# Kernel tuning notes

Hardware: AMD Instinct MI355X
Metric: run time of the kernel (lower is better)

The kernel has to match this reference:

```python
import jax, jax.numpy as jnp
import numpy as np

EMBED = 384; HEADS = 12; POINTS = 9; LAYERS = 2
KFG = 20; KBG = 50; NITER = 10
B = 4; H = 64; W = 64


def _layer_norm(x, g, b, eps=1e-5):
    m = x.mean(-1, keepdims=True)
    v = ((x - m) ** 2).mean(-1, keepdims=True)
    return (x - m) * jax.lax.rsqrt(v + eps) * g + b


def _sine_pos(pad, C):
    # pad [B,H,W], 1.0 = padded. SinePositionalEncoding(num_feats=C//2, normalize=True)
    nf = C // 2
    not_m = 1.0 - pad
    y = jnp.cumsum(not_m, axis=1)
    x = jnp.cumsum(not_m, axis=2)
    eps = 1e-6; sc = 2.0 * np.pi
    y = y / (y[:, -1:, :] + eps) * sc
    x = x / (x[:, :, -1:] + eps) * sc
    t = jnp.arange(nf, dtype=jnp.float32)
    dim_t = 10000.0 ** (2.0 * jnp.floor(t / 2.0) / nf)
    px = x[..., None] / dim_t
    py = y[..., None] / dim_t
    def inter(p):
        b_, h_, w_, _ = p.shape
        return jnp.stack((jnp.sin(p[..., 0::2]), jnp.cos(p[..., 1::2])), -1).reshape(b_, h_, w_, nf)
    pos = jnp.concatenate([inter(py), inter(px)], -1)  # [B,H,W,C]
    return pos.reshape(pad.shape[0], -1, C)


def _kmeans(x, w, K, n_iter):
    # masked Lloyd k-means. x [B,N,C], w [B,N] in {0,1} (1 = member of the group)
    Bq, N, C = x.shape
    score = w - (jnp.arange(N, dtype=x.dtype) / N) * 1e-3  # earliest in-group points first
    _, idx = jax.lax.top_k(score, K)
    centers = jnp.take_along_axis(x, idx[:, :, None], axis=1)  # [B,K,C]
    xsq = jnp.sum(x * x, -1)
    def body(i, c):
        d = xsq[:, :, None] - 2.0 * jnp.einsum('bnc,bkc->bnk', x, c) + jnp.sum(c * c, -1)[:, None, :]
        a = jax.nn.one_hot(jnp.argmin(d, -1), K, dtype=x.dtype) * w[:, :, None]
        num = jnp.einsum('bnk,bnc->bkc', a, x)
        den = jnp.sum(a, 1)[:, :, None]
        return jnp.where(den > 0, num / jnp.maximum(den, 1e-6), c)
    return jax.lax.fori_loop(0, n_iter, body, centers)


def _bilinear(value, loc, Hs, Ws):
    # value [B,heads,HW,hd]; loc [B,N,heads,P,2] normalized (x,y); zero padding outside
    Bq, nh, HW, hd = value.shape
    x = loc[..., 0] * Ws - 0.5
    y = loc[..., 1] * Hs - 0.5
    x0 = jnp.floor(x); y0 = jnp.floor(y)
    def tr(t):
        return jnp.transpose(t, (0, 2, 1, 3)).reshape(Bq, nh, -1)  # -> [B,heads,N*P]
    wx = tr(x - x0)[..., None]
    wy = tr(y - y0)[..., None]
    x0i = x0.astype(jnp.int32); y0i = y0.astype(jnp.int32)
    def gather(xi, yi):
        valid = (xi >= 0) & (xi < Ws) & (yi >= 0) & (yi < Hs)
        idx = jnp.clip(yi, 0, Hs - 1) * Ws + jnp.clip(xi, 0, Ws - 1)
        g = jnp.take_along_axis(value, tr(idx)[..., None], axis=2)  # [B,heads,N*P,hd]
        return g * tr(valid.astype(value.dtype))[..., None]
    v00 = gather(x0i, y0i)
    v01 = gather(x0i + 1, y0i)
    v10 = gather(x0i, y0i + 1)
    v11 = gather(x0i + 1, y0i + 1)
    out = v00 * (1 - wx) * (1 - wy) + v01 * wx * (1 - wy) + v10 * (1 - wx) * wy + v11 * wx * wy
    return out.reshape(Bq, nh, -1, POINTS, hd)  # [B,heads,N,P,hd]


def _forward(s_x, s_padding_mask, supp_mask, Wv, bv, Woff, boff, Wa, ba, Wout, bout,
             ln1_g, ln1_b, Wf1, Wf2, ln2_g, ln2_b):
    Bq, C, Hs, Ws = s_x.shape
    N = Hs * Ws
    hd = C // HEADS
    pad = (s_padding_mask[:, 0] == 255.0).astype(s_x.dtype)  # 1 = padded
    obj = (supp_mask[:, 0] == 1.0).astype(s_x.dtype)
    x = s_x.reshape(Bq, C, N).transpose(0, 2, 1)  # [B,N,C]
    padf = pad.reshape(Bq, N)
    objf = obj.reshape(Bq, N)
    # FG/BG k-means clustering of valid pixels (Cluster tool, n_iter=10)
    fg_c = _kmeans(x, objf * (1.0 - padf), KFG, NITER)
    bg_c = _kmeans(x, (1.0 - objf) * (1.0 - padf), KBG, NITER)
    pos = _sine_pos(pad, C)
    ry, rx = jnp.meshgrid(jnp.linspace(0.5, Hs - 0.5, Hs) / Hs,
                          jnp.linspace(0.5, Ws - 0.5, Ws) / Ws, indexing='ij')
    ref = jnp.stack([rx.reshape(-1), ry.reshape(-1)], -1)[None]  # [1,N,2] (x,y)
    wh = jnp.array([Ws, Hs], dtype=s_x.dtype)
    for l in range(LAYERS):
        q = x + pos
        v = (x * (1.0 - padf)[..., None]) @ Wv[l] + bv[l]
        v = v.reshape(Bq, N, HEADS, hd).transpose(0, 2, 1, 3)  # [B,heads,N,hd]
        off = (q @ Woff[l] + boff[l]).reshape(Bq, N, HEADS, POINTS, 2)
        aw = jax.nn.softmax((q @ Wa[l] + ba[l]).reshape(Bq, N, HEADS, POINTS), axis=-1)
        loc = ref[:, :, None, None, :] + off / wh
        samp = _bilinear(v, loc, Hs, Ws)  # [B,heads,N,P,hd]
        attn = jnp.einsum('bhnpd,bnhp->bnhd', samp, aw).reshape(Bq, N, C)
        x = _layer_norm(x + attn @ Wout[l] + bout[l], ln1_g[l], ln1_b[l])
        x = _layer_norm(x + jax.nn.relu(x @ Wf1[l]) @ Wf2[l], ln2_g[l], ln2_b[l])
    return jnp.concatenate([x, fg_c, bg_c], axis=1)  # [B, N+70, C]


def setup_inputs():
    key = jax.random.key(0)
    ks = jax.random.split(key, 12)
    dt = jnp.float32
    s = 0.02
    p = lambda k, shp: jax.random.normal(k, shp, dt) * s
    s_x = jax.random.normal(ks[0], (B, EMBED, H, W), dt)
    pad = jnp.zeros((B, 1, H, W), dt).at[:, :, :, W - 8:].set(255.0)  # right border padded
    supp_mask = (jax.random.uniform(ks[1], (B, 1, H, W)) < 0.15).astype(dt)
    return dict(
        s_x=s_x, s_padding_mask=pad, supp_mask=supp_mask,
        Wv=p(ks[2], (LAYERS, EMBED, EMBED)), bv=jnp.zeros((LAYERS, EMBED), dt),
        Woff=p(ks[3], (LAYERS, EMBED, HEADS * POINTS * 2)), boff=p(ks[4], (LAYERS, HEADS * POINTS * 2)),
        Wa=p(ks[5], (LAYERS, EMBED, HEADS * POINTS)), ba=jnp.zeros((LAYERS, HEADS * POINTS), dt),
        Wout=p(ks[6], (LAYERS, EMBED, EMBED)), bout=jnp.zeros((LAYERS, EMBED), dt),
        ln1_g=jnp.ones((LAYERS, EMBED), dt), ln1_b=jnp.zeros((LAYERS, EMBED), dt),
        Wf1=p(ks[7], (LAYERS, EMBED, 3 * EMBED)), Wf2=p(ks[8], (LAYERS, 3 * EMBED, EMBED)),
        ln2_g=jnp.ones((LAYERS, EMBED), dt), ln2_b=jnp.zeros((LAYERS, EMBED), dt))


def reference(s_x, s_padding_mask, supp_mask, Wv, bv, Woff, boff, Wa, ba, Wout, bout,
              ln1_g, ln1_b, Wf1, Wf2, ln2_g, ln2_b):
    return _forward(s_x, s_padding_mask, supp_mask, Wv, bv, Woff, boff, Wa, ba, Wout, bout,
                    ln1_g, ln1_b, Wf1, Wf2, ln2_g, ln2_b)
```

## Files before the change

kernel.cpp:

```cpp
#include <hip/hip_runtime.h>
#include <hip/hip_bf16.h>
#include <math.h>

#define NB 4
#define CE 384
#define NH 12
#define DH 32
#define NPTS 9
#define NLAYERS 2
#define KFG 20
#define KBG 50
#define NITER 10
#define HDIM 64
#define WDIM 64
#define NPIX 4096
#define BNTOT (NB * NPIX)
#define NROW (NPIX + KFG + KBG)
#define TWO_PI 6.283185307179586f

#define AS1 __attribute__((address_space(1)))
#define AS3 __attribute__((address_space(3)))

typedef __attribute__((ext_vector_type(8))) short short8;
typedef __attribute__((ext_vector_type(4))) float float4v;

static __device__ __forceinline__ unsigned short f2bf(float f) {
  __hip_bfloat16 h = __float2bfloat16(f);
  return *reinterpret_cast<unsigned short*>(&h);
}
static __device__ __forceinline__ float bf2f(unsigned short u) {
  unsigned x = ((unsigned)u) << 16;
  return __uint_as_float(x);
}

__device__ __forceinline__ float4 sample4(const float* __restrict__ vb, int xi, int yi, int c) {
  bool valid = (xi >= 0) & (xi < WDIM) & (yi >= 0) & (yi < HDIM);
  int xc = min(max(xi, 0), WDIM - 1), yc = min(max(yi, 0), HDIM - 1);
  float4 g = *(const float4*)(vb + (long)(yc * WDIM + xc) * CE + c);
  if (!valid) { g.x = 0.f; g.y = 0.f; g.z = 0.f; g.w = 0.f; }
  return g;
}

__global__ void k_masks(const float* __restrict__ pm, const float* __restrict__ sm,
                        float* padf, float* objf, float* notp, float* wfg, float* wbg) {
  int i = blockIdx.x * 256 + threadIdx.x;
  if (i >= NB * NPIX) return;
  float p  = (pm[i] == 255.0f) ? 1.f : 0.f;
  float o  = (sm[i] == 1.0f) ? 1.f : 0.f;
  float np_ = 1.f - p;
  padf[i] = p; objf[i] = o; notp[i] = np_;
  wfg[i] = o * np_;
  wbg[i] = (1.f - o) * np_;
}

__global__ __launch_bounds__(256) void k_transpose(const float* __restrict__ sx,
                                                   float* __restrict__ X) {
  __shared__ float tile[64][65];
  int nb = blockIdx.x * 64, cb = blockIdx.y * 64, b = blockIdx.z;
  int t = threadIdx.x;
  for (int idx = t; idx < 64 * 64; idx += 256) {
    int cc = idx >> 6, nn = idx & 63;
    tile[cc][nn] = sx[((long)b * CE + cb + cc) * NPIX + nb + nn];
  }
  __syncthreads();
  for (int idx = t; idx < 64 * 64; idx += 256) {
    int nn = idx >> 6, cc = idx & 63;
    X[((long)b * NPIX + nb + nn) * CE + cb + cc] = tile[cc][nn];
  }
}

__global__ void k_xsq(const float* __restrict__ X, double* __restrict__ xsq) {
  int row = blockIdx.x; int t = threadIdx.x;
  const float* xr = X + (long)row * CE;
  double s = 0.0;
  for (int i = t; i < CE; i += 64) { double v = (double)xr[i]; s += v * v; }
  #pragma unroll
  for (int o = 32; o > 0; o >>= 1) s += __shfl_down(s, o, 64);
  if (t == 0) xsq[row] = s;
}

__global__ __launch_bounds__(128) void k_cums(const float* __restrict__ padf,
                                              float* __restrict__ yvf,
                                              float* __restrict__ xvf,
                                              float* __restrict__ invdt) {
  __shared__ float pad_s[NPIX];
  int b = blockIdx.x; int t = threadIdx.x;
  for (int i = t; i < NPIX; i += 128) pad_s[i] = padf[b * NPIX + i];
  if (b == 0) {
    for (int c = t; c < CE; c += 128) {
      int tt = (c < 192) ? c : c - 192;
      invdt[c] = 1.0f / powf(10000.0f, (float)(2 * (tt / 2)) / 192.0f);
    }
  }
  __syncthreads();
  if (t < 64) {
    int w = t;
    float cum[64]; float tot = 0.f;
    for (int h = 0; h < 64; ++h) {
      float nm = 1.f - pad_s[h * WDIM + w];
      tot += nm; cum[h] = tot;
    }
    float sc = 1.f / (tot + 1e-6f);
    for (int h = 0; h < 64; ++h) yvf[b * NPIX + h * WDIM + w] = cum[h] * sc * TWO_PI;
  } else {
    int h = t - 64;
    float cum[64]; float tot = 0.f;
    for (int w = 0; w < 64; ++w) {
      float nm = 1.f - pad_s[h * WDIM + w];
      tot += nm; cum[w] = tot;
    }
    float sc = 1.f / (tot + 1e-6f);
    for (int w = 0; w < 64; ++w) xvf[b * NPIX + h * WDIM + w] = cum[w] * sc * TWO_PI;
  }
}

__global__ void k_kinit(const float* __restrict__ X, const float* __restrict__ wts,
                        double* __restrict__ cen, int K) {
  int b = blockIdx.x;
  __shared__ int idx[KBG];
  if (threadIdx.x == 0) {
    int cnt = 0;
    for (int n = 0; n < NPIX && cnt < K; ++n) if (wts[b * NPIX + n] > 0.f) idx[cnt++] = n;
    for (int n = 0; n < NPIX && cnt < K; ++n) if (!(wts[b * NPIX + n] > 0.f)) idx[cnt++] = n;
  }
  __syncthreads();
  for (int i = threadIdx.x; i < K * CE; i += blockDim.x) {
    int k = i / CE, c = i % CE;
    cen[((long)b * K + k) * CE + c] = (double)X[((long)b * NPIX + idx[k]) * CE + c];
  }
}

__global__ __launch_bounds__(256) void k_dots(
    const float* __restrict__ X, const double* __restrict__ xsq,
    const double* __restrict__ cenF, const double* __restrict__ cenB,
    double* __restrict__ candD, int* __restrict__ candI, int* __restrict__ cntAll) {
  __shared__ double ct[10][CE];
  __shared__ double csq_s[10];
  int z = blockIdx.y;
  int isBg = (z >= 2) ? 1 : 0;
  int k0 = isBg ? (z - 2) * 10 : z * 10;
  int t = threadIdx.x;
  int n = blockIdx.x * 256 + t;
  int b = blockIdx.x >> 4;
  if (blockIdx.x == 0 && z == 0) {
    for (int i = t; i < NB * (KFG + KBG); i += 256) cntAll[i] = 0;
  }
  const double* cb = (isBg ? cenB + (long)b * KBG * CE
                           : cenF + (long)b * KFG * CE) + (long)k0 * CE;
  for (int i = t; i < 10 * CE; i += 256) ct[i / CE][i % CE] = cb[i];
  __syncthreads();
  if (t < 64) {
    for (int kk = 0; kk < 10; ++kk) {
      double s = 0.0;
      for (int c = t; c < CE; c += 64) { double v = ct[kk][c]; s += v * v; }
      #pragma unroll
      for (int o = 32; o > 0; o >>= 1) s += __shfl_down(s, o, 64);
      if (t == 0) csq_s[kk] = s;
    }
  }
  __syncthreads();
  const float* xr = X + (long)n * CE;
  double acc[10];
  #pragma unroll
  for (int k = 0; k < 10; ++k) acc[k] = 0.0;
  for (int c0 = 0; c0 < CE; c0 += 8) {
    double xd[8];
    float4 u = *(const float4*)(xr + c0);
    float4 v = *(const float4*)(xr + c0 + 4);
    xd[0] = u.x; xd[1] = u.y; xd[2] = u.z; xd[3] = u.w;
    xd[4] = v.x; xd[5] = v.y; xd[6] = v.z; xd[7] = v.w;
    #pragma unroll
    for (int k = 0; k < 10; ++k) {
      #pragma unroll
      for (int j = 0; j < 8; j += 2) {
        double2 cv = *(const double2*)(&ct[k][c0 + j]);
        acc[k] += xd[j] * cv.x;
        acc[k] += xd[j + 1] * cv.y;
      }
    }
  }
  double q = xsq[n];
  double best = 1.0e300; int bi = 0;
  #pragma unroll
  for (int k = 0; k < 10; ++k) {
    double d = q - 2.0 * acc[k] + csq_s[k];
    if (d < best) { best = d; bi = k0 + k; }
  }
  long gi = (long)z * BNTOT + n;
  candD[gi] = best;
  candI[gi] = bi;
}

__global__ void k_asn(const double* __restrict__ candD, const int* __restrict__ candI,
                      const float* __restrict__ wfg, const float* __restrict__ wbg,
                      int* __restrict__ listF, int* __restrict__ listB,
                      int* __restrict__ cntAll) {
  int n = blockIdx.x * 256 + threadIdx.x;
  if (n >= BNTOT) return;
  int b = n >> 12;
  int nn = n & (NPIX - 1);
  float wf = wfg[n], wb = wbg[n];
  if (wf > 0.f) {
    double d0 = candD[n]; int i0 = candI[n];
    double d1 = candD[(long)BNTOT + n];
    if (d1 < d0) { d0 = d1; i0 = candI[(long)BNTOT + n]; }
    int slot = atomicAdd(&cntAll[b * KFG + i0], 1);
    listF[((long)b * KFG + i0) * NPIX + slot] = nn;
  } else if (wb > 0.f) {
    double d0 = candD[2L * BNTOT + n]; int i0 = candI[2L * BNTOT + n];
    #pragma unroll
    for (int z = 3; z < 7; ++z) {
      double dz = candD[(long)z * BNTOT + n];
      if (dz < d0) { d0 = dz; i0 = candI[(long)z * BNTOT + n]; }
    }
    int slot = atomicAdd(&cntAll[NB * KFG + b * KBG + i0], 1);
    listB[((long)b * KBG + i0) * NPIX + slot] = nn;
  }
}

__global__ __launch_bounds__(128) void k_cacc(
    const float* __restrict__ X,
    const int* __restrict__ listF, const int* __restrict__ listB,
    const int* __restrict__ cntAll,
    const double* __restrict__ srcF, double* __restrict__ dstF,
    const double* __restrict__ srcB, double* __restrict__ dstB) {
  __shared__ int ls[NPIX];
  int slice = blockIdx.x;
  int kq = blockIdx.y;
  int b = blockIdx.z;
  int t = threadIdx.x;
  int c = slice * 128 + t;
  const int* list; int cnt; const double* src; double* dst; long o;
  if (kq < KFG) {
    cnt = cntAll[b * KFG + kq];
    list = listF + ((long)b * KFG + kq) * NPIX;
    o = ((long)b * KFG + kq) * CE + c;
    src = srcF; dst = dstF;
  } else {
    int k = kq - KFG;
    cnt = cntAll[NB * KFG + b * KBG + k];
    list = listB + ((long)b * KBG + k) * NPIX;
    o = ((long)b * KBG + k) * CE + c;
    src = srcB; dst = dstB;
  }
  for (int i = t; i < cnt; i += 128) ls[i] = list[i];
  __syncthreads();
  const float* Xb = X + (long)b * NPIX * CE;
  double acc = 0.0;
  int i = 0;
  for (; i + 4 <= cnt; i += 4) {
    int n0 = ls[i], n1 = ls[i + 1], n2 = ls[i + 2], n3 = ls[i + 3];
    float v0 = Xb[(long)n0 * CE + c];
    float v1 = Xb[(long)n1 * CE + c];
    float v2 = Xb[(long)n2 * CE + c];
    float v3 = Xb[(long)n3 * CE + c];
    acc += (double)v0; acc += (double)v1; acc += (double)v2; acc += (double)v3;
  }
  for (; i < cnt; ++i) acc += (double)Xb[(long)ls[i] * CE + c];
  dst[o] = (cnt > 0) ? (acc / (double)cnt) : src[o];
}

__global__ void k_cvtQV(const float* __restrict__ X,
                        const float* __restrict__ yvf, const float* __restrict__ xvf,
                        const float* __restrict__ invdt, const float* __restrict__ notp,
                        float* __restrict__ POS,
                        unsigned short* __restrict__ QB, unsigned short* __restrict__ VBin) {
  long i = (long)blockIdx.x * 256 + threadIdx.x;
  if (i >= (long)NB * NPIX * CE) return;
  int c = (int)(i % CE);
  long row = i / CE;
  float p = (c < 192) ? yvf[row] : xvf[row];
  float v = p * invdt[c];
  int tt = (c < 192) ? c : c - 192;
  float r = (tt & 1) ? cosf(v) : sinf(v);
  POS[i] = r;
  float x = X[i];
  QB[i] = f2bf(x + r);
  VBin[i] = f2bf(x * notp[row]);
}

__global__ void k_cvtW_all(
    const float* __restrict__ Wv_l, const float* __restrict__ Woff_l,
    const float* __restrict__ Wa_l, const float* __restrict__ Wout_l,
    const float* __restrict__ Wf1_l, const float* __restrict__ Wf2_l,
    const float* __restrict__ boff_l, const float* __restrict__ ba_l,
    unsigned short* __restrict__ W0, unsigned short* __restrict__ W1,
    unsigned short* __restrict__ W3, unsigned short* __restrict__ W4,
    unsigned short* __restrict__ W5, float* __restrict__ biasCat) {
  int i = blockIdx.x * 256 + threadIdx.x;
  const int S = 147456, SF = 442368;
  if (i < S) {
    int n = i / 384, k = i % 384;
    W0[i] = f2bf(Wv_l[(long)k * 384 + n]);
  } else if (i < 2 * S) {
    int j = i - S; int n = j / 384, k = j % 384;
    float v = 0.f;
    if (n < 216) v = Woff_l[(long)k * 216 + n];
    else if (n < 324) v = Wa_l[(long)k * 108 + (n - 216)];
    W1[j] = f2bf(v);
  } else if (i < 3 * S) {
    int j = i - 2 * S; int n = j / 384, k = j % 384;
    W3[j] = f2bf(Wout_l[(long)k * 384 + n]);
  } else if (i < 3 * S + SF) {
    int j = i - 3 * S; int n = j / 384, k = j % 384;
    W4[j] = f2bf(Wf1_l[(long)k * 1152 + n]);
  } else if (i < 3 * S + 2 * SF) {
    int j = i - 3 * S - SF; int n = j / 1152, k = j % 1152;
    W5[j] = f2bf(Wf2_l[(long)k * 384 + n]);
  } else if (i < 3 * S + 2 * SF + 324) {
    int j = i - 3 * S - 2 * SF;
    biasCat[j] = (j < 216) ? boff_l[j] : ba_l[j - 216];
  }
}

__global__ __launch_bounds__(256) void k_gemm_bf(
    const unsigned short* __restrict__ A, const unsigned short* __restrict__ Bt,
    const float* __restrict__ bias, float* __restrict__ Cf, unsigned short* __restrict__ Cb,
    int M, int K, int N, int relu) {
  __shared__ unsigned short As[128 * 32];
  __shared__ unsigned short Bs[128 * 32];
  int m0 = blockIdx.y * 128, n0 = blockIdx.x * 128;
  int t = threadIdx.x;
  int w = t >> 6, l = t & 63;
  int wm = w >> 1, wn = w & 1;
  int half = l >> 4, lr = l & 15;
  float4v acc[4][4] = {};
  for (int k0 = 0; k0 < K; k0 += 32) {
    #pragma unroll
    for (int i = 0; i < 2; ++i) {
      int c = w * 64 + i * 256 + l;
      int r = c >> 2, part = c & 3;
      int ldsOff = (w * 64 + i * 256) * 8;
      __builtin_amdgcn_global_load_lds(
          (const AS1 unsigned int*)(A + (size_t)(m0 + r) * K + k0 + part * 8),
          (AS3 unsigned int*)(As + ldsOff), 16, 0, 0);
      __builtin_amdgcn_global_load_lds(
          (const AS1 unsigned int*)(Bt + (size_t)(n0 + r) * K + k0 + part * 8),
          (AS3 unsigned int*)(Bs + ldsOff), 16, 0, 0);
    }
    __syncthreads();
    short8 af[4], bfr[4];
    #pragma unroll
    for (int am = 0; am < 4; ++am)
      af[am] = *(const short8*)(&As[(wm * 64 + am * 16 + lr) * 32 + half * 8]);
    #pragma unroll
    for (int bn = 0; bn < 4; ++bn)
      bfr[bn] = *(const short8*)(&Bs[(wn * 64 + bn * 16 + lr) * 32 + half * 8]);
    #pragma unroll
    for (int am = 0; am < 4; ++am)
      #pragma unroll
      for (int bn = 0; bn < 4; ++bn)
        acc[am][bn] = __builtin_amdgcn_mfma_f32_16x16x32_bf16(af[am], bfr[bn], acc[am][bn], 0, 0, 0);
    __syncthreads();
  }
  #pragma unroll
  for (int am = 0; am < 4; ++am) {
    #pragma unroll
    for (int bn = 0; bn < 4; ++bn) {
      int gc = n0 + wn * 64 + bn * 16 + lr;
      if (gc < N) {
        float bv = bias ? bias[gc] : 0.f;
        int gr0 = m0 + wm * 64 + am * 16 + half * 4;
        #pragma unroll
        for (int r = 0; r < 4; ++r) {
          float v = acc[am][bn][r] + bv;
          if (relu) v = fmaxf(v, 0.f);
          size_t oi = (size_t)(gr0 + r) * N + gc;
          if (Cf) Cf[oi] = v;
          else Cb[oi] = f2bf(v);
        }
      }
    }
  }
}

__global__ void k_coords(const unsigned short* __restrict__ OAB, float4* __restrict__ CRD) {
  int idx = blockIdx.x * 256 + threadIdx.x;
  if (idx >= NB * NPIX * NH) return;
  int row = idx / NH, h = idx % NH;
  int n = row & (NPIX - 1);
  int hh = n >> 6, ww = n & 63;
  float refx = ((float)ww + 0.5f) / (float)WDIM;
  float refy = ((float)hh + 0.5f) / (float)HDIM;
  const unsigned short* oab = OAB + (size_t)row * 324;
  float f[NPTS];
  #pragma unroll
  for (int j = 0; j < NPTS; ++j) f[j] = bf2f(oab[216 + h * 9 + j]);
  float m = f[0];
  #pragma unroll
  for (int j = 1; j < NPTS; ++j) m = fmaxf(m, f[j]);
  float s = 0.f;
  #pragma unroll
  for (int j = 0; j < NPTS; ++j) { f[j] = expf(f[j] - m); s += f[j]; }
  float inv = 1.f / s;
  float4* crd = CRD + (size_t)row * 108 + h * 9;
  #pragma unroll
  for (int p = 0; p < NPTS; ++p) {
    float ox = bf2f(oab[h * 18 + p * 2 + 0]);
    float oy = bf2f(oab[h * 18 + p * 2 + 1]);
    float lx = refx + ox / (float)WDIM;
    float ly = refy + oy / (float)HDIM;
    float xs = lx * (float)WDIM - 0.5f;
    float ys = ly * (float)HDIM - 0.5f;
    float x0f = floorf(xs), y0f = floorf(ys);
    int x0 = (int)x0f, y0 = (int)y0f;
    float4 o;
    o.x = xs - x0f;
    o.y = ys - y0f;
    o.z = f[p] * inv;
    o.w = __int_as_float((y0 << 16) | (x0 & 0xFFFF));
    crd[p] = o;
  }
}

__global__ __launch_bounds__(256) void k_gather(
    const float* __restrict__ V, const float4* __restrict__ CRD,
    uint2* __restrict__ ATTu) {
  int idx = blockIdx.x * 256 + threadIdx.x;
  if (idx >= NB * NPIX * (CE / 4)) return;
  int row = idx / (CE / 4), cq = idx % (CE / 4);
  int c = cq * 4;
  int h = c >> 5;
  int b = row >> 12;
  const float* vb = V + (size_t)b * NPIX * CE;
  const float4* crd = CRD + (size_t)row * 108 + h * 9;
  float a0 = 0.f, a1 = 0.f, a2 = 0.f, a3 = 0.f;
  #pragma unroll
  for (int p = 0; p < NPTS; ++p) {
    float4 o = crd[p];
    int pk = __float_as_int(o.w);
    int x0 = (int)(short)(pk & 0xFFFF);
    int y0 = pk >> 16;
    float wx = o.x, wy = o.y, aw = o.z;
    float4 g00 = sample4(vb, x0,     y0,     c);
    float4 g01 = sample4(vb, x0 + 1, y0,     c);
    float4 g10 = sample4(vb, x0,     y0 + 1, c);
    float4 g11 = sample4(vb, x0 + 1, y0 + 1, c);
    float w00 = (1.f - wx) * (1.f - wy), w01 = wx * (1.f - wy);
    float w10 = (1.f - wx) * wy,         w11 = wx * wy;
    a0 += aw * (g00.x * w00 + g01.x * w01 + g10.x * w10 + g11.x * w11);
    a1 += aw * (g00.y * w00 + g01.y * w01 + g10.y * w10 + g11.y * w11);
    a2 += aw * (g00.z * w00 + g01.z * w01 + g10.z * w10 + g11.z * w11);
    a3 += aw * (g00.w * w00 + g01.w * w01 + g10.w * w10 + g11.w * w11);
  }
  uint2 pk2;
  pk2.x = (unsigned)f2bf(a0) | ((unsigned)f2bf(a1) << 16);
  pk2.y = (unsigned)f2bf(a2) | ((unsigned)f2bf(a3) << 16);
  ATTu[(size_t)row * (CE / 4) + cq] = pk2;
}

__global__ __launch_bounds__(256) void k_ln(
    float* __restrict__ X, const float* __restrict__ T,
    const float* __restrict__ g, const float* __restrict__ bb,
    unsigned short* __restrict__ xbOut,
    const float* __restrict__ posp, const float* __restrict__ notp,
    unsigned short* __restrict__ qb, unsigned short* __restrict__ vbin,
    float* __restrict__ outp) {
  int t = threadIdx.x;
  int row = blockIdx.x * 4 + (t >> 6);
  int lane = t & 63;
  float* xr = X + (long)row * CE;
  const float* tr = T + (long)row * CE;
  float v[6]; float s = 0.f;
  #pragma unroll
  for (int i = 0; i < 6; ++i) { v[i] = xr[lane + 64 * i] + tr[lane + 64 * i]; s += v[i]; }
  #pragma unroll
  for (int o = 32; o > 0; o >>= 1) s += __shfl_down(s, o, 64);
  s = __shfl(s, 0, 64);
  float m = s / (float)CE;
  float var = 0.f;
  #pragma unroll
  for (int i = 0; i < 6; ++i) { float d = v[i] - m; var += d * d; }
  #pragma unroll
  for (int o = 32; o > 0; o >>= 1) var += __shfl_down(var, o, 64);
  var = __shfl(var, 0, 64);
  float rst = rsqrtf(var / (float)CE + 1e-5f);
  float nprow = notp ? notp[row] : 0.f;
  int b = row >> 12, n = row & (NPIX - 1);
  #pragma unroll
  for (int i = 0; i < 6; ++i) {
    int c = lane + 64 * i;
    float xn = (v[i] - m) * rst * g[c] + bb[c];
    if (outp) outp[((long)b * NROW + n) * CE + c] = xn;
    else xr[c] = xn;
    if (xbOut) xbOut[(long)row * CE + c] = f2bf(xn);
    if (qb) {
      qb[(long)row * CE + c] = f2bf(xn + posp[(long)row * CE + c]);
      vbin[(long)row * CE + c] = f2bf(xn * nprow);
    }
  }
}

__global__ void k_out_cen(const double* __restrict__ fg, const double* __restrict__ bg,
                          float* __restrict__ out) {
  int i = blockIdx.x * 256 + threadIdx.x;
  const int tot = NB * (KFG + KBG) * CE;
  if (i >= tot) return;
  int c = i % CE;
  int r = i / CE;
  int rr = r % (KFG + KBG);
  int b = r / (KFG + KBG);
  float v;
  if (rr < KFG) v = (float)fg[((long)b * KFG + rr) * CE + c];
  else v = (float)bg[((long)b * KBG + (rr - KFG)) * CE + c];
  out[((long)b * NROW + NPIX + rr) * CE + c] = v;
}

extern "C" void kernel_launch(void* const* d_in, const int* in_sizes, int n_in,
                              void* d_out, int out_size, void* d_ws, size_t ws_size,
                              hipStream_t stream) {
  (void)in_sizes; (void)n_in; (void)out_size; (void)ws_size;
  const float* s_x  = (const float*)d_in[0];
  const float* s_pm = (const float*)d_in[1];
  const float* s_sm = (const float*)d_in[2];
  const float* Wv   = (const float*)d_in[3];
  const float* bv   = (const float*)d_in[4];
  const float* Woff = (const float*)d_in[5];
  const float* boff = (const float*)d_in[6];
  const float* Wa   = (const float*)d_in[7];
  const float* ba   = (const float*)d_in[8];
  const float* Wout = (const float*)d_in[9];
  const float* bout = (const float*)d_in[10];
  const float* ln1g = (const float*)d_in[11];
  const float* ln1b = (const float*)d_in[12];
  const float* Wf1  = (const float*)d_in[13];
  const float* Wf2  = (const float*)d_in[14];
  const float* ln2g = (const float*)d_in[15];
  const float* ln2b = (const float*)d_in[16];
  float* out = (float*)d_out;
  char* pb = (char*)d_ws;

  const long BN  = (long)NB * NPIX;
  const long BNC = BN * CE;

  float* X    = (float*)pb; pb += BNC * 4;
  float* POS  = (float*)pb; pb += BNC * 4;
  float* V    = (float*)pb; pb += BNC * 4;
  float* T2   = (float*)pb; pb += BNC * 4;
  unsigned short* QB   = (unsigned short*)pb; pb += BNC * 2;
  unsigned short* VBin = (unsigned short*)pb; pb += BNC * 2;
  unsigned short* T1b  = (unsigned short*)pb; pb += BNC * 2;
  unsigned short* Zbf  = QB;
  unsigned short* XB   = (unsigned short*)pb; pb += BNC * 2;
  unsigned short* OAB  = (unsigned short*)pb; pb += BN * 324 * 2;
  float4* CRD = (float4*)pb; pb += BN * 108 * 16;
  const int S_W = 147456, S_F = 442368;
  unsigned short* WT[NLAYERS][5];
  float* biasCat[NLAYERS];
  for (int l = 0; l < NLAYERS; ++l) {
    WT[l][0] = (unsigned short*)pb; pb += S_W * 2;
    WT[l][1] = (unsigned short*)pb; pb += S_W * 2;
    WT[l][2] = (unsigned short*)pb; pb += S_W * 2;
    WT[l][3] = (unsigned short*)pb; pb += S_F * 2;
    WT[l][4] = (unsigned short*)pb; pb += S_F * 2;
    biasCat[l] = (float*)pb; pb += 324 * 4;
  }
  float* padf = (float*)pb; pb += BN * 4;
  float* objf = (float*)pb; pb += BN * 4;
  float* notp = (float*)pb; pb += BN * 4;
  float* wfg  = (float*)pb; pb += BN * 4;
  float* wbg  = (float*)pb; pb += BN * 4;
  float* yvf  = (float*)pb; pb += BN * 4;
  float* xvf  = (float*)pb; pb += BN * 4;
  float* invdt = (float*)pb; pb += CE * 4;
  pb = (char*)(((size_t)pb + 7) & ~(size_t)7);
  double* xsq   = (double*)pb; pb += BN * 8;
  double* candD = (double*)pb; pb += BN * 7 * 8;
  double* cFgA = (double*)pb; pb += (long)NB * KFG * CE * 8;
  double* cFgB = (double*)pb; pb += (long)NB * KFG * CE * 8;
  double* cBgA = (double*)pb; pb += (long)NB * KBG * CE * 8;
  double* cBgB = (double*)pb; pb += (long)NB * KBG * CE * 8;
  int* candI  = (int*)pb; pb += BN * 7 * 4;
  int* cntAll = (int*)pb; pb += NB * (KFG + KBG) * 4;
  int* listF  = (int*)pb; pb += (long)NB * KFG * NPIX * 4;
  int* listB  = (int*)pb; pb += (long)NB * KBG * NPIX * 4;

  int bn = (int)BN;
  int cvtBlocks = (int)((BNC + 255) / 256);

  k_masks<<<(bn + 255) / 256, 256, 0, stream>>>(s_pm, s_sm, padf, objf, notp, wfg, wbg);
  k_transpose<<<dim3(NPIX / 64, CE / 64, NB), 256, 0, stream>>>(s_x, X);
  k_xsq<<<bn, 64, 0, stream>>>(X, xsq);
  k_cums<<<NB, 128, 0, stream>>>(padf, yvf, xvf, invdt);
  k_cvtQV<<<cvtBlocks, 256, 0, stream>>>(X, yvf, xvf, invdt, notp, POS, QB, VBin);

  const int CVTW_TOT = 3 * S_W + 2 * S_F + 324;
  for (int l = 0; l < NLAYERS; ++l) {
    k_cvtW_all<<<(CVTW_TOT + 255) / 256, 256, 0, stream>>>(
        Wv + (long)l * CE * CE, Woff + (long)l * CE * 216, Wa + (long)l * CE * 108,
        Wout + (long)l * CE * CE, Wf1 + (long)l * CE * 1152, Wf2 + (long)l * 1152 * CE,
        boff + l * 216, ba + l * 108,
        WT[l][0], WT[l][1], WT[l][2], WT[l][3], WT[l][4], biasCat[l]);
  }

  double *srcF = cFgA, *dstF = cFgB, *srcB = cBgA, *dstB = cBgB;
  k_kinit<<<NB, 256, 0, stream>>>(X, wfg, srcF, KFG);
  k_kinit<<<NB, 256, 0, stream>>>(X, wbg, srcB, KBG);
  for (int it = 0; it < NITER; ++it) {
    k_dots<<<dim3(bn / 256, 7), 256, 0, stream>>>(X, xsq, srcF, srcB, candD, candI, cntAll);
    k_asn<<<(bn + 255) / 256, 256, 0, stream>>>(candD, candI, wfg, wbg, listF, listB, cntAll);
    k_cacc<<<dim3(3, KFG + KBG, NB), 128, 0, stream>>>(
        X, listF, listB, cntAll, srcF, dstF, srcB, dstB);
    double* tmp;
    tmp = srcF; srcF = dstF; dstF = tmp;
    tmp = srcB; srcB = dstB; dstB = tmp;
  }
  double* fgC = srcF; double* bgC = srcB;

  for (int l = 0; l < NLAYERS; ++l) {
    const float* bv_l   = bv   + l * CE;
    const float* bout_l = bout + l * CE;
    int last = (l == NLAYERS - 1);

    k_gemm_bf<<<dim3(3, 128), 256, 0, stream>>>(VBin, WT[l][0], bv_l, V, (unsigned short*)nullptr,
                                                bn, CE, 384, 0);
    k_gemm_bf<<<dim3(3, 128), 256, 0, stream>>>(QB, WT[l][1], biasCat[l], (float*)nullptr, OAB,
                                                bn, CE, 324, 0);
    k_coords<<<(bn * NH + 255) / 256, 256, 0, stream>>>(OAB, CRD);
    k_gather<<<(bn * (CE / 4) + 255) / 256, 256, 0, stream>>>(V, CRD, (uint2*)T1b);
    k_gemm_bf<<<dim3(3, 128), 256, 0, stream>>>(T1b, WT[l][2], bout_l, T2, (unsigned short*)nullptr,
                                                bn, CE, 384, 0);
    k_ln<<<bn / 4, 256, 0, stream>>>(X, T2, ln1g + l * CE, ln1b + l * CE,
                                     XB, (const float*)nullptr, (const float*)nullptr,
                                     (unsigned short*)nullptr, (unsigned short*)nullptr,
                                     (float*)nullptr);
    k_gemm_bf<<<dim3(9, 128), 256, 0, stream>>>(XB, WT[l][3], (const float*)nullptr,
                                                (float*)nullptr, Zbf, bn, CE, 1152, 1);
    k_gemm_bf<<<dim3(3, 128), 256, 0, stream>>>(Zbf, WT[l][4], (const float*)nullptr,
                                                T2, (unsigned short*)nullptr, bn, 1152, 384, 0);
    if (!last) {
      k_ln<<<bn / 4, 256, 0, stream>>>(X, T2, ln2g + l * CE, ln2b + l * CE,
                                       (unsigned short*)nullptr, POS, notp, QB, VBin,
                                       (float*)nullptr);
    } else {
      k_ln<<<bn / 4, 256, 0, stream>>>(X, T2, ln2g + l * CE, ln2b + l * CE,
                                       (unsigned short*)nullptr, (const float*)nullptr,
                                       (const float*)nullptr, (unsigned short*)nullptr,
                                       (unsigned short*)nullptr, out);
    }
  }

  k_out_cen<<<(NB * (KFG + KBG) * CE + 255) / 256, 256, 0, stream>>>(fgC, bgC, out);
}
```

Measured before the change: 1.484 ms.

## Split k-means distance dot products across four lanes per point

The k-means distance kernel now gives each point four threads, each covering a quarter of the channels, and combines the partial sums with cross-lane shuffles. The grid grows fourfold, so more blocks are in flight and each thread walks a shorter serial double-precision chain. The shared center tile is padded per quarter (stride 98) to reduce LDS bank conflicts, and the center norms are read straight from global memory. The cost is reloading the center tile in four times as many blocks, plus shuffle overhead.

After: 1.601 ms. 7.9% more time.

```diff
diff --git a/kernel.cpp b/kernel.cpp
--- a/kernel.cpp
+++ b/kernel.cpp
@@ -130,40 +130,47 @@
   }
 }
 
+#define HSTR 98
+#define KSTR 392
+
 __global__ __launch_bounds__(256) void k_dots(
     const float* __restrict__ X, const double* __restrict__ xsq,
     const double* __restrict__ cenF, const double* __restrict__ cenB,
     double* __restrict__ candD, int* __restrict__ candI, int* __restrict__ cntAll) {
-  __shared__ double ct[10][CE];
+  __shared__ double ct[10 * KSTR];
   __shared__ double csq_s[10];
   int z = blockIdx.y;
   int isBg = (z >= 2) ? 1 : 0;
   int k0 = isBg ? (z - 2) * 10 : z * 10;
   int t = threadIdx.x;
-  int n = blockIdx.x * 256 + t;
-  int b = blockIdx.x >> 4;
+  int h = t & 3;
+  int n = blockIdx.x * 64 + (t >> 2);
+  int b = blockIdx.x >> 6;
   if (blockIdx.x == 0 && z == 0) {
     for (int i = t; i < NB * (KFG + KBG); i += 256) cntAll[i] = 0;
   }
   const double* cb = (isBg ? cenB + (long)b * KBG * CE
                            : cenF + (long)b * KFG * CE) + (long)k0 * CE;
-  for (int i = t; i < 10 * CE; i += 256) ct[i / CE][i % CE] = cb[i];
-  __syncthreads();
+  for (int i = t; i < 10 * CE; i += 256) {
+    int k = i / CE, c = i % CE;
+    ct[k * KSTR + (c / 96) * HSTR + (c % 96)] = cb[i];
+  }
   if (t < 64) {
     for (int kk = 0; kk < 10; ++kk) {
       double s = 0.0;
-      for (int c = t; c < CE; c += 64) { double v = ct[kk][c]; s += v * v; }
+      for (int c = t; c < CE; c += 64) { double v = cb[kk * CE + c]; s += v * v; }
       #pragma unroll
       for (int o = 32; o > 0; o >>= 1) s += __shfl_down(s, o, 64);
       if (t == 0) csq_s[kk] = s;
     }
   }
   __syncthreads();
-  const float* xr = X + (long)n * CE;
+  const float* xr = X + (long)n * CE + h * 96;
+  const double* cth = ct + h * HSTR;
   double acc[10];
   #pragma unroll
   for (int k = 0; k < 10; ++k) acc[k] = 0.0;
-  for (int c0 = 0; c0 < CE; c0 += 8) {
+  for (int c0 = 0; c0 < 96; c0 += 8) {
     double xd[8];
     float4 u = *(const float4*)(xr + c0);
     float4 v = *(const float4*)(xr + c0 + 4);
@@ -173,22 +180,31 @@
     for (int k = 0; k < 10; ++k) {
       #pragma unroll
       for (int j = 0; j < 8; j += 2) {
-        double2 cv = *(const double2*)(&ct[k][c0 + j]);
+        double2 cv = *(const double2*)(&cth[k * KSTR + c0 + j]);
         acc[k] += xd[j] * cv.x;
         acc[k] += xd[j + 1] * cv.y;
       }
     }
   }
-  double q = xsq[n];
-  double best = 1.0e300; int bi = 0;
   #pragma unroll
   for (int k = 0; k < 10; ++k) {
-    double d = q - 2.0 * acc[k] + csq_s[k];
-    if (d < best) { best = d; bi = k0 + k; }
-  }
-  long gi = (long)z * BNTOT + n;
-  candD[gi] = best;
-  candI[gi] = bi;
+    double a = acc[k];
+    a += __shfl_xor(a, 1, 64);
+    a += __shfl_xor(a, 2, 64);
+    acc[k] = a;
+  }
+  if (h == 0) {
+    double q = xsq[n];
+    double best = 1.0e300; int bi = 0;
+    #pragma unroll
+    for (int k = 0; k < 10; ++k) {
+      double d = q - 2.0 * acc[k] + csq_s[k];
+      if (d < best) { best = d; bi = k0 + k; }
+    }
+    long gi = (long)z * BNTOT + n;
+    candD[gi] = best;
+    candI[gi] = bi;
+  }
 }
 
 __global__ void k_asn(const double* __restrict__ candD, const int* __restrict__ candI,
@@ -597,7 +613,7 @@
   k_kinit<<<NB, 256, 0, stream>>>(X, wfg, srcF, KFG);
   k_kinit<<<NB, 256, 0, stream>>>(X, wbg, srcB, KBG);
   for (int it = 0; it < NITER; ++it) {
-    k_dots<<<dim3(bn / 256, 7), 256, 0, stream>>>(X, xsq, srcF, srcB, candD, candI, cntAll);
+    k_dots<<<dim3(bn / 64, 7), 256, 0, stream>>>(X, xsq, srcF, srcB, candD, candI, cntAll);
     k_asn<<<(bn + 255) / 256, 256, 0, stream>>>(candD, candI, wfg, wbg, listF, listB, cntAll);
     k_cacc<<<dim3(3, KFG + KBG, NB), 128, 0, stream>>>(
         X, listF, listB, cntAll, srcF, dstF, srcB, dstB);
```
